# Kernel tuning notes

Hardware: AMD Instinct MI355X
Metric: run time of the kernel (lower is better)

The kernel has to match this reference:

```python
import jax, jax.numpy as jnp
import numpy as np

D_MODEL = 512
N_HEADS = 8
B, S = 4, 1024
REL_HIDDEN = 64


def setup_inputs() -> dict:
    key = jax.random.key(0)
    ks = jax.random.split(key, 16)

    def g(k, shape, scale=0.02):
        return jax.random.normal(k, shape, dtype=jnp.float32) * scale

    x = jax.random.normal(ks[0], (B, S, D_MODEL), dtype=jnp.float32)
    freqs = jax.random.uniform(ks[1], (B, S, 1), dtype=jnp.float32)
    return {
        "x": x,
        "freqs": freqs,
        "Wq": g(ks[2], (D_MODEL, D_MODEL)), "bq": g(ks[3], (D_MODEL,)),
        "Wk": g(ks[4], (D_MODEL, D_MODEL)), "bk": g(ks[5], (D_MODEL,)),
        "Wv": g(ks[6], (D_MODEL, D_MODEL)), "bv": g(ks[7], (D_MODEL,)),
        "Wo": g(ks[8], (D_MODEL, D_MODEL)), "bo": g(ks[9], (D_MODEL,)),
        "W1": g(ks[10], (2, REL_HIDDEN)), "b1": g(ks[11], (REL_HIDDEN,)),
        "W2": g(ks[12], (REL_HIDDEN, N_HEADS)), "b2": g(ks[13], (N_HEADS,)),
    }


def reference(x, freqs, Wq, bq, Wk, bk, Wv, bv, Wo, bo, W1, b1, W2, b2):
    b, s, d = x.shape
    h = N_HEADS
    dh = d // h

    def proj(W, bias):  # (b,s,d) -> (b,h,s,dh)
        return (x @ W + bias).reshape(b, s, h, dh).transpose(0, 2, 1, 3)

    Q = proj(Wq, bq)
    K = proj(Wk, bk)
    V = proj(Wv, bv)

    scores = jnp.einsum('bhid,bhjd->bhij', Q, K) / jnp.sqrt(jnp.float32(dh))

    # per-pair relative-frequency features: (b,s,s,2)
    eps = 1e-6
    fd = freqs[:, :, None, :] - freqs[:, None, :, :]
    fr = jnp.log((freqs[:, :, None, :] + eps) / (freqs[:, None, :, :] + eps))
    rel = jnp.concatenate([fd, fr], axis=-1)

    # MLP bias -> (b,s,s,h) -> (b,h,s,s)
    bias = jax.nn.relu(rel @ W1 + b1) @ W2 + b2
    scores = scores + jnp.transpose(bias, (0, 3, 1, 2))

    attn = jax.nn.softmax(scores, axis=-1)
    ctx = jnp.einsum('bhij,bhjd->bhid', attn, V)
    ctx = ctx.transpose(0, 2, 1, 3).reshape(b, s, d)
    return ctx @ Wo + bo
```

## Files before the change

### kernel.cpp

```cpp
#include <hip/hip_runtime.h>
#include <hip/hip_bf16.h>
#include <cstdint>

#define BATCH   4
#define SEQ     1024
#define DM      512
#define NH      8
#define DH      64
#define RH      64

typedef float f32x4 __attribute__((ext_vector_type(4)));
typedef __bf16 bf16x8 __attribute__((ext_vector_type(8)));

#define QB_OFF    (0)
#define KB_OFF    (4  << 20)
#define VT_OFF    (8  << 20)
#define XB_OFF    (12 << 20)
#define WT_OFF    (16 << 20)
#define WOT_OFF   (18 << 20)
#define W2T_OFF   (19 << 20)
#define AW_OFF    (20 << 20)
#define CW_OFF    (21 << 20)
#define CTXB_OFF  (22 << 20)
#define BIAS_OFF  (32 << 20)

__global__ __launch_bounds__(256) void cast_x(
    const float* __restrict__ x, __bf16* __restrict__ xb)
{
    const size_t i = ((size_t)blockIdx.x * 256 + threadIdx.x) * 8;
    const float4 a = *(const float4*)&x[i];
    const float4 b = *(const float4*)&x[i + 4];
    bf16x8 o;
    o[0] = (__bf16)a.x; o[1] = (__bf16)a.y; o[2] = (__bf16)a.z; o[3] = (__bf16)a.w;
    o[4] = (__bf16)b.x; o[5] = (__bf16)b.y; o[6] = (__bf16)b.z; o[7] = (__bf16)b.w;
    *(bf16x8*)&xb[i] = o;
}

__global__ __launch_bounds__(256) void cast_w(
    const float* __restrict__ Wq, const float* __restrict__ Wk,
    const float* __restrict__ Wv, const float* __restrict__ Wo,
    __bf16* __restrict__ Wt, __bf16* __restrict__ Wot)
{
    const int t = threadIdx.x;
    const int k0 = blockIdx.x * 64;
    const int n0 = blockIdx.y * 64;
    const int z  = blockIdx.z;
    const float* __restrict__ src = (z == 0) ? Wq : (z == 1) ? Wk : (z == 2) ? Wv : Wo;
    __bf16* __restrict__ dst = (z < 3) ? (Wt + (size_t)(z * 512 + n0) * 512)
                                       : (Wot + (size_t)n0 * 512);

    __shared__ __align__(16) float Ts[64][65];
    #pragma unroll
    for (int i = 0; i < 4; ++i) {
        const int id = t + i * 256;
        const int row = id >> 4, c4 = (id & 15) * 4;
        const float4 v = *(const float4*)&src[(size_t)(k0 + row) * DM + n0 + c4];
        Ts[row][c4 + 0] = v.x; Ts[row][c4 + 1] = v.y;
        Ts[row][c4 + 2] = v.z; Ts[row][c4 + 3] = v.w;
    }
    __syncthreads();
    #pragma unroll
    for (int i = 0; i < 2; ++i) {
        const int id = t + i * 256;
        const int rn = id >> 3, ck = (id & 7) * 8;
        bf16x8 o;
        #pragma unroll
        for (int j = 0; j < 8; ++j) o[j] = (__bf16)Ts[ck + j][rn];
        *(bf16x8*)&dst[(size_t)rn * 512 + k0 + ck] = o;
    }
}

__global__ __launch_bounds__(256) void w2t_kernel(
    const float* __restrict__ W2, __bf16* __restrict__ W2t)
{
    const int t = threadIdx.x;
    #pragma unroll
    for (int r = 0; r < 4; ++r) {
        const int id = t + r * 256;
        const int h = id >> 6, k = id & 63;
        W2t[id] = (h < NH) ? (__bf16)W2[k * NH + h] : (__bf16)0.f;
    }
}

__global__ __launch_bounds__(256) void gemm_qkv_mfma(
    const __bf16* __restrict__ xb, const __bf16* __restrict__ Wt,
    const float* __restrict__ bq, const float* __restrict__ bk,
    const float* __restrict__ bv,
    __bf16* __restrict__ Qb, __bf16* __restrict__ Kb, __bf16* __restrict__ Vtb)
{
    const int t = threadIdx.x;
    const int wave = t >> 6, lane = t & 63;
    const int wm = wave >> 1, wn = wave & 1;
    const int r = lane & 15, kc = lane >> 4, q4 = kc * 4;
    const int lin = blockIdx.y * 12 + blockIdx.x;
    const int swz = (lin & 7) * 48 + (lin >> 3);
    const int m0 = (swz / 12) * 128;
    const int n0 = (swz % 12) * 128;
    const int sec = n0 >> 9;
    const int nn = n0 & 511;

    __shared__ __align__(16) char smem[36864];
    __bf16* __restrict__ As = (__bf16*)smem;
    __bf16* __restrict__ Bs = (__bf16*)(smem + 18432);

    f32x4 acc[4][4];
    #pragma unroll
    for (int i = 0; i < 4; ++i)
        #pragma unroll
        for (int j = 0; j < 4; ++j) acc[i][j] = {0.f, 0.f, 0.f, 0.f};

    const int srow = t >> 3, sck = (t & 7) * 8;
    const __bf16* __restrict__ Ag = xb + (size_t)(m0 + srow) * 512 + sck;
    const __bf16* __restrict__ Bg = Wt + (size_t)(n0 + srow) * 512 + sck;

    for (int k0 = 0; k0 < 512; k0 += 64) {
        bf16x8 ra[4], rb[4];
        #pragma unroll
        for (int i = 0; i < 4; ++i) {
            ra[i] = *(const bf16x8*)(Ag + (size_t)i * 32 * 512 + k0);
            rb[i] = *(const bf16x8*)(Bg + (size_t)i * 32 * 512 + k0);
        }
        __syncthreads();
        #pragma unroll
        for (int i = 0; i < 4; ++i) {
            *(bf16x8*)&As[(srow + i * 32) * 72 + sck] = ra[i];
            *(bf16x8*)&Bs[(srow + i * 32) * 72 + sck] = rb[i];
        }
        __syncthreads();
        #pragma unroll
        for (int ks = 0; ks < 2; ++ks) {
            bf16x8 af[4], bf[4];
            #pragma unroll
            for (int mf = 0; mf < 4; ++mf)
                af[mf] = *(const bf16x8*)&As[(wm * 64 + mf * 16 + r) * 72 + ks * 32 + kc * 8];
            #pragma unroll
            for (int nf = 0; nf < 4; ++nf)
                bf[nf] = *(const bf16x8*)&Bs[(wn * 64 + nf * 16 + r) * 72 + ks * 32 + kc * 8];
            #pragma unroll
            for (int mf = 0; mf < 4; ++mf)
                #pragma unroll
                for (int nf = 0; nf < 4; ++nf)
                    acc[mf][nf] = __builtin_amdgcn_mfma_f32_16x16x32_bf16(
                        af[mf], bf[nf], acc[mf][nf], 0, 0, 0);
        }
    }

    const float* __restrict__ bias = (sec == 0) ? bq : (sec == 1) ? bk : bv;
    __syncthreads();
    __bf16* __restrict__ Ls = (__bf16*)smem;
    if (sec < 2) {
        #pragma unroll
        for (int mf = 0; mf < 4; ++mf)
            #pragma unroll
            for (int nf = 0; nf < 4; ++nf) {
                const int n_l = wn * 64 + nf * 16 + r;
                const float bb = bias[nn + n_l];
                #pragma unroll
                for (int rr = 0; rr < 4; ++rr)
                    Ls[(wm * 64 + mf * 16 + q4 + rr) * 136 + n_l] =
                        (__bf16)(acc[mf][nf][rr] + bb);
            }
    } else {
        #pragma unroll
        for (int mf = 0; mf < 4; ++mf)
            #pragma unroll
            for (int nf = 0; nf < 4; ++nf) {
                const int n_l = wn * 64 + nf * 16 + r;
                const float bb = bias[nn + n_l];
                #pragma unroll
                for (int rr = 0; rr < 4; ++rr)
                    Ls[n_l * 136 + (wm * 64 + mf * 16 + q4 + rr)] =
                        (__bf16)(acc[mf][nf][rr] + bb);
            }
    }
    __syncthreads();

    const int b = m0 >> 10, sbase = m0 & 1023;
    if (sec < 2) {
        __bf16* __restrict__ dst = sec ? Kb : Qb;
        #pragma unroll
        for (int i = 0; i < 8; ++i) {
            const int id = t + i * 256;
            const int row = id >> 4, nc = (id & 15) * 8;
            const bf16x8 v = *(const bf16x8*)&Ls[row * 136 + nc];
            const int ng = nn + nc, h = ng >> 6, c = ng & 63;
            *(bf16x8*)&dst[((size_t)(b * NH + h) * SEQ + sbase + row) * DH + c] = v;
        }
    } else {
        #pragma unroll
        for (int i = 0; i < 8; ++i) {
            const int id = t + i * 256;
            const int nrow = id >> 4, mc = (id & 15) * 8;
            const bf16x8 v = *(const bf16x8*)&Ls[nrow * 136 + mc];
            const int ng = nn + nrow, h = ng >> 6, c = ng & 63;
            *(bf16x8*)&Vtb[((size_t)(b * NH + h) * DH + c) * SEQ + sbase + mc] = v;
        }
    }
}

__global__ __launch_bounds__(256) void gemm_out_mfma(
    const __bf16* __restrict__ ctxb, const __bf16* __restrict__ Wot,
    const float* __restrict__ bo, float* __restrict__ out)
{
    const int t = threadIdx.x;
    const int wave = t >> 6, lane = t & 63;
    const int wm = wave >> 1, wn = wave & 1;
    const int r = lane & 15, kc = lane >> 4, q4 = kc * 4;
    const int lin = blockIdx.y * 4 + blockIdx.x;
    const int swz = (lin & 7) * 16 + (lin >> 3);
    const int m0 = (swz / 4) * 128;
    const int n0 = (swz % 4) * 128;

    __shared__ __align__(16) char smem[36864];
    __bf16* __restrict__ As = (__bf16*)smem;
    __bf16* __restrict__ Bs = (__bf16*)(smem + 18432);

    f32x4 acc[4][4];
    #pragma unroll
    for (int i = 0; i < 4; ++i)
        #pragma unroll
        for (int j = 0; j < 4; ++j) acc[i][j] = {0.f, 0.f, 0.f, 0.f};

    const int srow = t >> 3, sck = (t & 7) * 8;
    const __bf16* __restrict__ Ag = ctxb + (size_t)(m0 + srow) * 512 + sck;
    const __bf16* __restrict__ Bg = Wot + (size_t)(n0 + srow) * 512 + sck;

    for (int k0 = 0; k0 < 512; k0 += 64) {
        bf16x8 ra[4], rb[4];
        #pragma unroll
        for (int i = 0; i < 4; ++i) {
            ra[i] = *(const bf16x8*)(Ag + (size_t)i * 32 * 512 + k0);
            rb[i] = *(const bf16x8*)(Bg + (size_t)i * 32 * 512 + k0);
        }
        __syncthreads();
        #pragma unroll
        for (int i = 0; i < 4; ++i) {
            *(bf16x8*)&As[(srow + i * 32) * 72 + sck] = ra[i];
            *(bf16x8*)&Bs[(srow + i * 32) * 72 + sck] = rb[i];
        }
        __syncthreads();
        #pragma unroll
        for (int ks = 0; ks < 2; ++ks) {
            bf16x8 af[4], bf[4];
            #pragma unroll
            for (int mf = 0; mf < 4; ++mf)
                af[mf] = *(const bf16x8*)&As[(wm * 64 + mf * 16 + r) * 72 + ks * 32 + kc * 8];
            #pragma unroll
            for (int nf = 0; nf < 4; ++nf)
                bf[nf] = *(const bf16x8*)&Bs[(wn * 64 + nf * 16 + r) * 72 + ks * 32 + kc * 8];
            #pragma unroll
            for (int mf = 0; mf < 4; ++mf)
                #pragma unroll
                for (int nf = 0; nf < 4; ++nf)
                    acc[mf][nf] = __builtin_amdgcn_mfma_f32_16x16x32_bf16(
                        af[mf], bf[nf], acc[mf][nf], 0, 0, 0);
        }
    }

    #pragma unroll
    for (int mf = 0; mf < 4; ++mf)
        #pragma unroll
        for (int nf = 0; nf < 4; ++nf) {
            const int n_l = wn * 64 + nf * 16 + r;
            const float bb = bo[n0 + n_l];
            #pragma unroll
            for (int rr = 0; rr < 4; ++rr)
                out[(size_t)(m0 + wm * 64 + mf * 16 + q4 + rr) * DM + n0 + n_l] =
                    acc[mf][nf][rr] + bb;
        }
}

__global__ __launch_bounds__(64) void rel_kernel(
    const float* __restrict__ freqs,
    const float* __restrict__ W1,
    const float* __restrict__ b1,
    float* __restrict__ Aw,
    float* __restrict__ Cw)
{
    const int row = blockIdx.x;
    const int k = threadIdx.x;
    const float f = freqs[row];
    const float L = logf(f + 1e-6f);
    const float base = f * W1[k] + L * W1[RH + k];
    Aw[(size_t)row * RH + k] = base + b1[k];
    Cw[(size_t)row * RH + k] = -base;
}

__global__ __launch_bounds__(256) void bias_mfma(
    const float* __restrict__ Aw, const float* __restrict__ Cw,
    const __bf16* __restrict__ W2t, __bf16* __restrict__ biasb)
{
    const int t = threadIdx.x;
    const int wave = t >> 6, lane = t & 63;
    const int jl = lane & 15, kc = lane >> 4;
    const int j0 = blockIdx.x * 128;
    const int i0 = blockIdx.y * 16;
    const int b  = blockIdx.z;

    __shared__ __align__(16) float Cs[128][68];

    {
        const int jr = t >> 1, half = (t & 1) * 32;
        const float* __restrict__ src = &Cw[((size_t)b * SEQ + j0 + jr) * RH + half];
        #pragma unroll
        for (int q = 0; q < 8; ++q) {
            const float4 v = *(const float4*)(src + q * 4);
            *(float4*)&Cs[jr][half + q * 4] = v;
        }
    }

    const bf16x8 w2f0 = *(const bf16x8*)&W2t[jl * 64 + kc * 8];
    const bf16x8 w2f1 = *(const bf16x8*)&W2t[jl * 64 + 32 + kc * 8];

    __syncthreads();

    const int iw = i0 + wave * 4;
    #pragma unroll
    for (int ii = 0; ii < 4; ++ii) {
        const int i = iw + ii;
        const float* __restrict__ ap = &Aw[((size_t)b * SEQ + i) * RH];
        const float4 a0 = *(const float4*)(ap + kc * 8);
        const float4 a1 = *(const float4*)(ap + kc * 8 + 4);
        const float4 a2 = *(const float4*)(ap + 32 + kc * 8);
        const float4 a3 = *(const float4*)(ap + 32 + kc * 8 + 4);

        #pragma unroll
        for (int jt = 0; jt < 8; ++jt) {
            const float* __restrict__ cp = &Cs[jt * 16 + jl][kc * 8];
            f32x4 acc = {0.f, 0.f, 0.f, 0.f};

            const float4 c0 = *(const float4*)(cp);
            const float4 c1 = *(const float4*)(cp + 4);
            bf16x8 hb0;
            hb0[0] = (__bf16)fmaxf(a0.x + c0.x, 0.f);
            hb0[1] = (__bf16)fmaxf(a0.y + c0.y, 0.f);
            hb0[2] = (__bf16)fmaxf(a0.z + c0.z, 0.f);
            hb0[3] = (__bf16)fmaxf(a0.w + c0.w, 0.f);
            hb0[4] = (__bf16)fmaxf(a1.x + c1.x, 0.f);
            hb0[5] = (__bf16)fmaxf(a1.y + c1.y, 0.f);
            hb0[6] = (__bf16)fmaxf(a1.z + c1.z, 0.f);
            hb0[7] = (__bf16)fmaxf(a1.w + c1.w, 0.f);
            acc = __builtin_amdgcn_mfma_f32_16x16x32_bf16(w2f0, hb0, acc, 0, 0, 0);

            const float4 c2 = *(const float4*)(cp + 32);
            const float4 c3 = *(const float4*)(cp + 36);
            bf16x8 hb1;
            hb1[0] = (__bf16)fmaxf(a2.x + c2.x, 0.f);
            hb1[1] = (__bf16)fmaxf(a2.y + c2.y, 0.f);
            hb1[2] = (__bf16)fmaxf(a2.z + c2.z, 0.f);
            hb1[3] = (__bf16)fmaxf(a2.w + c2.w, 0.f);
            hb1[4] = (__bf16)fmaxf(a3.x + c3.x, 0.f);
            hb1[5] = (__bf16)fmaxf(a3.y + c3.y, 0.f);
            hb1[6] = (__bf16)fmaxf(a3.z + c3.z, 0.f);
            hb1[7] = (__bf16)fmaxf(a3.w + c3.w, 0.f);
            acc = __builtin_amdgcn_mfma_f32_16x16x32_bf16(w2f1, hb1, acc, 0, 0, 0);

            if (kc < 2) {
                #pragma unroll
                for (int rr = 0; rr < 4; ++rr)
                    biasb[(((size_t)b * NH + kc * 4 + rr) * SEQ + i) * SEQ
                          + j0 + jt * 16 + jl] = (__bf16)acc[rr];
            }
        }
    }
}

#define PSTR 1032

__global__ __launch_bounds__(512) void attn_mfma(
    const __bf16* __restrict__ Qb, const __bf16* __restrict__ Kb,
    const __bf16* __restrict__ Vtb, const __bf16* __restrict__ biasb,
    __bf16* __restrict__ ctxb)
{
    const int t = threadIdx.x;
    const int wave = t >> 6, lane = t & 63;
    const int r = lane & 15, kc = lane >> 4;
    const int blk = (blockIdx.x & 7) * 256 + (blockIdx.x >> 3);
    const int it = blk & 63;
    const int h  = (blk >> 6) & 7;
    const int b  = blk >> 9;
    const int s0 = it * 16;
    const int bh = b * NH + h;

    __shared__ __align__(16) __bf16 Pb[16 * PSTR];
    __shared__ __align__(16) float part[1088];
    __shared__ float red[8][16];
    __shared__ float invl[16];

    uint32_t brg[4][8];
    {
        const uint16_t* __restrict__ bb = (const uint16_t*)biasb
            + ((size_t)bh * SEQ + s0 + kc * 4) * SEQ + wave * 128 + r;
        #pragma unroll
        for (int rr = 0; rr < 4; ++rr)
            #pragma unroll
            for (int jt = 0; jt < 8; ++jt)
                brg[rr][jt] = bb[(size_t)rr * SEQ + jt * 16];
    }

    f32x4 sc[8];
    {
        const __bf16* __restrict__ Qp = Qb + ((size_t)bh * SEQ + s0) * DH;
        const __bf16* __restrict__ Kp = Kb + ((size_t)bh * SEQ + wave * 128) * DH;
        const bf16x8 qa0 = *(const bf16x8*)(Qp + r * DH + kc * 8);
        const bf16x8 qa1 = *(const bf16x8*)(Qp + r * DH + 32 + kc * 8);
        __builtin_amdgcn_s_setprio(1);
        #pragma unroll
        for (int jt = 0; jt < 8; ++jt) {
            const bf16x8 kb0 = *(const bf16x8*)(Kp + (size_t)(jt * 16 + r) * DH + kc * 8);
            const bf16x8 kb1 = *(const bf16x8*)(Kp + (size_t)(jt * 16 + r) * DH + 32 + kc * 8);
            f32x4 a = {0.f, 0.f, 0.f, 0.f};
            a = __builtin_amdgcn_mfma_f32_16x16x32_bf16(qa0, kb0, a, 0, 0, 0);
            a = __builtin_amdgcn_mfma_f32_16x16x32_bf16(qa1, kb1, a, 0, 0, 0);
            sc[jt] = a;
        }
        __builtin_amdgcn_s_setprio(0);
    }

    float psum[4] = {0.f, 0.f, 0.f, 0.f};
    #pragma unroll
    for (int jt = 0; jt < 8; ++jt) {
        #pragma unroll
        for (int rr = 0; rr < 4; ++rr) {
            const float s = fmaf(sc[jt][rr], 0.125f,
                                 __uint_as_float(brg[rr][jt] << 16));
            const float p = __expf(fminf(s, 30.f));
            sc[jt][rr] = p;
            psum[rr] += p;
        }
    }
    #pragma unroll
    for (int mask = 8; mask >= 1; mask >>= 1)
        #pragma unroll
        for (int rr = 0; rr < 4; ++rr)
            psum[rr] += __shfl_xor(psum[rr], mask);
    if (r == 0) {
        #pragma unroll
        for (int rr = 0; rr < 4; ++rr) red[wave][kc * 4 + rr] = psum[rr];
    }
    #pragma unroll
    for (int jt = 0; jt < 8; ++jt)
        #pragma unroll
        for (int rr = 0; rr < 4; ++rr)
            Pb[(kc * 4 + rr) * PSTR + wave * 128 + jt * 16 + r] = (__bf16)sc[jt][rr];
    __syncthreads();

    if (t < 16) {
        float l = 0.f;
        #pragma unroll
        for (int w = 0; w < 8; ++w) l += red[w][t];
        invl[t] = 1.0f / l;
    }

    {
        const int ct = wave & 3, kh = wave >> 2;
        const __bf16* __restrict__ Vp =
            Vtb + ((size_t)bh * DH + ct * 16 + r) * SEQ + kh * 512;
        f32x4 acc = {0.f, 0.f, 0.f, 0.f};
        __builtin_amdgcn_s_setprio(1);
        #pragma unroll 4
        for (int jt = 0; jt < 16; ++jt) {
            const bf16x8 pa = *(const bf16x8*)&Pb[r * PSTR + kh * 512 + jt * 32 + kc * 8];
            const bf16x8 vb = *(const bf16x8*)(Vp + jt * 32 + kc * 8);
            acc = __builtin_amdgcn_mfma_f32_16x16x32_bf16(pa, vb, acc, 0, 0, 0);
        }
        __builtin_amdgcn_s_setprio(0);
        if (kh == 1) {
            #pragma unroll
            for (int rr = 0; rr < 4; ++rr)
                part[ct * 272 + (kc * 4 + rr) * 17 + r] = acc[rr];
        }
        __syncthreads();
        if (kh == 0) {
            #pragma unroll
            for (int rr = 0; rr < 4; ++rr) {
                const int row = kc * 4 + rr;
                const float v = (acc[rr] + part[ct * 272 + row * 17 + r]) * invl[row];
                ctxb[((size_t)(b * SEQ) + s0 + row) * DM + h * DH + ct * 16 + r] = (__bf16)v;
            }
        }
    }
}

extern "C" void kernel_launch(void* const* d_in, const int* in_sizes, int n_in,
                              void* d_out, int out_size, void* d_ws, size_t ws_size,
                              hipStream_t stream)
{
    const float* x     = (const float*)d_in[0];
    const float* freqs = (const float*)d_in[1];
    const float* Wq    = (const float*)d_in[2];
    const float* bq    = (const float*)d_in[3];
    const float* Wk    = (const float*)d_in[4];
    const float* bk    = (const float*)d_in[5];
    const float* Wv    = (const float*)d_in[6];
    const float* bv    = (const float*)d_in[7];
    const float* Wo    = (const float*)d_in[8];
    const float* bo    = (const float*)d_in[9];
    const float* W1    = (const float*)d_in[10];
    const float* b1    = (const float*)d_in[11];
    const float* W2    = (const float*)d_in[12];

    char* wsb = (char*)d_ws;
    __bf16* Qb    = (__bf16*)(wsb + QB_OFF);
    __bf16* Kb    = (__bf16*)(wsb + KB_OFF);
    __bf16* Vtb   = (__bf16*)(wsb + VT_OFF);
    __bf16* xb    = (__bf16*)(wsb + XB_OFF);
    __bf16* Wt    = (__bf16*)(wsb + WT_OFF);
    __bf16* Wot   = (__bf16*)(wsb + WOT_OFF);
    __bf16* W2t   = (__bf16*)(wsb + W2T_OFF);
    float*  Aw    = (float*)(wsb + AW_OFF);
    float*  Cw    = (float*)(wsb + CW_OFF);
    __bf16* ctxb  = (__bf16*)(wsb + CTXB_OFF);
    __bf16* biasb = (__bf16*)(wsb + BIAS_OFF);
    float* out = (float*)d_out;

    cast_x<<<dim3(1024), 256, 0, stream>>>(x, xb);
    cast_w<<<dim3(8, 8, 4), 256, 0, stream>>>(Wq, Wk, Wv, Wo, Wt, Wot);
    w2t_kernel<<<dim3(1), 256, 0, stream>>>(W2, W2t);
    rel_kernel<<<dim3(4096), 64, 0, stream>>>(freqs, W1, b1, Aw, Cw);
    gemm_qkv_mfma<<<dim3(12, 32), 256, 0, stream>>>(xb, Wt, bq, bk, bv, Qb, Kb, Vtb);
    bias_mfma<<<dim3(8, 64, 4), 256, 0, stream>>>(Aw, Cw, W2t, biasb);
    attn_mfma<<<dim3(2048), 512, 0, stream>>>(Qb, Kb, Vtb, biasb, ctxb);
    gemm_out_mfma<<<dim3(4, 32), 256, 0, stream>>>(ctxb, Wot, bo, out);
}
```

Measured before the change: 219.2 us.

## Tile attention over 64 query rows with chunked key loop and double-buffered P

Each attention block now handles 64 query rows (4 query groups across waves) instead of 16, walking the 1024 keys in four 256-wide chunks. Per chunk it builds exp scores into a double-buffered LDS tile and does the P·V MFMAs right away, keeping the output accumulators in registers. This removes the cross-wave partial-sum exchange and lets each K/V tile serve four times as many queries, cutting global K/V traffic. The cost is four times fewer blocks (512) and a barrier per chunk, which may lower occupancy and latency hiding.

```diff
diff --git a/kernel.cpp b/kernel.cpp
--- a/kernel.cpp
+++ b/kernel.cpp
@@ -365,7 +365,7 @@
     }
 }
 
-#define PSTR 1032
+#define PCH 264
 
 __global__ __launch_bounds__(512) void attn_mfma(
     const __bf16* __restrict__ Qb, const __bf16* __restrict__ Kb,
@@ -373,62 +373,95 @@
     __bf16* __restrict__ ctxb)
 {
     const int t = threadIdx.x;
-    const int wave = t >> 6, lane = t & 63;
+    const int w = t >> 6, lane = t & 63;
     const int r = lane & 15, kc = lane >> 4;
-    const int blk = (blockIdx.x & 7) * 256 + (blockIdx.x >> 3);
-    const int it = blk & 63;
-    const int h  = (blk >> 6) & 7;
-    const int b  = blk >> 9;
-    const int s0 = it * 16;
+    const int qg = w & 3, jh = w >> 2;
+    const int blk = (blockIdx.x & 7) * 64 + (blockIdx.x >> 3);
+    const int it = blk & 15;
+    const int h  = (blk >> 4) & 7;
+    const int b  = blk >> 7;
+    const int s0 = it * 64;
     const int bh = b * NH + h;
 
-    __shared__ __align__(16) __bf16 Pb[16 * PSTR];
-    __shared__ __align__(16) float part[1088];
+    __shared__ __align__(16) __bf16 Pb[2][64 * PCH];
     __shared__ float red[8][16];
-    __shared__ float invl[16];
-
-    uint32_t brg[4][8];
-    {
-        const uint16_t* __restrict__ bb = (const uint16_t*)biasb
-            + ((size_t)bh * SEQ + s0 + kc * 4) * SEQ + wave * 128 + r;
-        #pragma unroll
-        for (int rr = 0; rr < 4; ++rr)
-            #pragma unroll
-            for (int jt = 0; jt < 8; ++jt)
-                brg[rr][jt] = bb[(size_t)rr * SEQ + jt * 16];
-    }
-
-    f32x4 sc[8];
-    {
-        const __bf16* __restrict__ Qp = Qb + ((size_t)bh * SEQ + s0) * DH;
-        const __bf16* __restrict__ Kp = Kb + ((size_t)bh * SEQ + wave * 128) * DH;
-        const bf16x8 qa0 = *(const bf16x8*)(Qp + r * DH + kc * 8);
-        const bf16x8 qa1 = *(const bf16x8*)(Qp + r * DH + 32 + kc * 8);
-        __builtin_amdgcn_s_setprio(1);
+
+    const __bf16* __restrict__ Qp = Qb + ((size_t)bh * SEQ + s0 + qg * 16) * DH;
+    const bf16x8 qa0 = *(const bf16x8*)(Qp + r * DH + kc * 8);
+    const bf16x8 qa1 = *(const bf16x8*)(Qp + r * DH + 32 + kc * 8);
+
+    float psum[4] = {0.f, 0.f, 0.f, 0.f};
+    f32x4 oacc0 = {0.f, 0.f, 0.f, 0.f};
+    f32x4 oacc1 = {0.f, 0.f, 0.f, 0.f};
+
+    const __bf16* __restrict__ KpBase = Kb + (size_t)bh * SEQ * DH;
+    const uint16_t* __restrict__ bbBase = (const uint16_t*)biasb
+        + ((size_t)bh * SEQ + s0 + qg * 16 + kc * 4) * SEQ + jh * 128 + r;
+
+    for (int c = 0; c < 4; ++c) {
+        uint32_t brg[4][8];
+        {
+            const uint16_t* __restrict__ bb = bbBase + c * 256;
+            #pragma unroll
+            for (int rr = 0; rr < 4; ++rr)
+                #pragma unroll
+                for (int jt = 0; jt < 8; ++jt)
+                    brg[rr][jt] = bb[(size_t)rr * SEQ + jt * 16];
+        }
+
+        f32x4 sc[8];
+        {
+            const __bf16* __restrict__ Kp =
+                KpBase + (size_t)(c * 256 + jh * 128) * DH;
+            __builtin_amdgcn_s_setprio(1);
+            #pragma unroll
+            for (int jt = 0; jt < 8; ++jt) {
+                const bf16x8 kb0 = *(const bf16x8*)(Kp + (size_t)(jt * 16 + r) * DH + kc * 8);
+                const bf16x8 kb1 = *(const bf16x8*)(Kp + (size_t)(jt * 16 + r) * DH + 32 + kc * 8);
+                f32x4 a = {0.f, 0.f, 0.f, 0.f};
+                a = __builtin_amdgcn_mfma_f32_16x16x32_bf16(qa0, kb0, a, 0, 0, 0);
+                a = __builtin_amdgcn_mfma_f32_16x16x32_bf16(qa1, kb1, a, 0, 0, 0);
+                sc[jt] = a;
+            }
+            __builtin_amdgcn_s_setprio(0);
+        }
+
+        __bf16* __restrict__ P = Pb[c & 1];
         #pragma unroll
         for (int jt = 0; jt < 8; ++jt) {
-            const bf16x8 kb0 = *(const bf16x8*)(Kp + (size_t)(jt * 16 + r) * DH + kc * 8);
-            const bf16x8 kb1 = *(const bf16x8*)(Kp + (size_t)(jt * 16 + r) * DH + 32 + kc * 8);
-            f32x4 a = {0.f, 0.f, 0.f, 0.f};
-            a = __builtin_amdgcn_mfma_f32_16x16x32_bf16(qa0, kb0, a, 0, 0, 0);
-            a = __builtin_amdgcn_mfma_f32_16x16x32_bf16(qa1, kb1, a, 0, 0, 0);
-            sc[jt] = a;
-        }
-        __builtin_amdgcn_s_setprio(0);
-    }
-
-    float psum[4] = {0.f, 0.f, 0.f, 0.f};
-    #pragma unroll
-    for (int jt = 0; jt < 8; ++jt) {
-        #pragma unroll
-        for (int rr = 0; rr < 4; ++rr) {
-            const float s = fmaf(sc[jt][rr], 0.125f,
-                                 __uint_as_float(brg[rr][jt] << 16));
-            const float p = __expf(fminf(s, 30.f));
-            sc[jt][rr] = p;
-            psum[rr] += p;
-        }
-    }
+            #pragma unroll
+            for (int rr = 0; rr < 4; ++rr) {
+                const float s = fmaf(sc[jt][rr], 0.125f,
+                                     __uint_as_float(brg[rr][jt] << 16));
+                const float p = __expf(fminf(s, 30.f));
+                psum[rr] += p;
+                P[(qg * 16 + kc * 4 + rr) * PCH + jh * 128 + jt * 16 + r] = (__bf16)p;
+            }
+        }
+        __syncthreads();
+
+        {
+            const __bf16* __restrict__ Pr = Pb[c & 1] + (qg * 16 + r) * PCH;
+            __builtin_amdgcn_s_setprio(1);
+            #pragma unroll
+            for (int cc = 0; cc < 2; ++cc) {
+                const int crow = (jh * 2 + cc) * 16 + r;
+                const __bf16* __restrict__ Vp =
+                    Vtb + ((size_t)bh * DH + crow) * SEQ + c * 256;
+                #pragma unroll
+                for (int jt = 0; jt < 8; ++jt) {
+                    const bf16x8 pa = *(const bf16x8*)(Pr + jt * 32 + kc * 8);
+                    const bf16x8 vb = *(const bf16x8*)(Vp + jt * 32 + kc * 8);
+                    if (cc == 0)
+                        oacc0 = __builtin_amdgcn_mfma_f32_16x16x32_bf16(pa, vb, oacc0, 0, 0, 0);
+                    else
+                        oacc1 = __builtin_amdgcn_mfma_f32_16x16x32_bf16(pa, vb, oacc1, 0, 0, 0);
+                }
+            }
+            __builtin_amdgcn_s_setprio(0);
+        }
+    }
+
     #pragma unroll
     for (int mask = 8; mask >= 1; mask >>= 1)
         #pragma unroll
@@ -436,49 +469,19 @@
             psum[rr] += __shfl_xor(psum[rr], mask);
     if (r == 0) {
         #pragma unroll
-        for (int rr = 0; rr < 4; ++rr) red[wave][kc * 4 + rr] = psum[rr];
-    }
-    #pragma unroll
-    for (int jt = 0; jt < 8; ++jt)
-        #pragma unroll
-        for (int rr = 0; rr < 4; ++rr)
-            Pb[(kc * 4 + rr) * PSTR + wave * 128 + jt * 16 + r] = (__bf16)sc[jt][rr];
+        for (int rr = 0; rr < 4; ++rr) red[w][kc * 4 + rr] = psum[rr];
+    }
     __syncthreads();
 
-    if (t < 16) {
-        float l = 0.f;
-        #pragma unroll
-        for (int w = 0; w < 8; ++w) l += red[w][t];
-        invl[t] = 1.0f / l;
-    }
-
-    {
-        const int ct = wave & 3, kh = wave >> 2;
-        const __bf16* __restrict__ Vp =
-            Vtb + ((size_t)bh * DH + ct * 16 + r) * SEQ + kh * 512;
-        f32x4 acc = {0.f, 0.f, 0.f, 0.f};
-        __builtin_amdgcn_s_setprio(1);
-        #pragma unroll 4
-        for (int jt = 0; jt < 16; ++jt) {
-            const bf16x8 pa = *(const bf16x8*)&Pb[r * PSTR + kh * 512 + jt * 32 + kc * 8];
-            const bf16x8 vb = *(const bf16x8*)(Vp + jt * 32 + kc * 8);
-            acc = __builtin_amdgcn_mfma_f32_16x16x32_bf16(pa, vb, acc, 0, 0, 0);
-        }
-        __builtin_amdgcn_s_setprio(0);
-        if (kh == 1) {
-            #pragma unroll
-            for (int rr = 0; rr < 4; ++rr)
-                part[ct * 272 + (kc * 4 + rr) * 17 + r] = acc[rr];
-        }
-        __syncthreads();
-        if (kh == 0) {
-            #pragma unroll
-            for (int rr = 0; rr < 4; ++rr) {
-                const int row = kc * 4 + rr;
-                const float v = (acc[rr] + part[ct * 272 + row * 17 + r]) * invl[row];
-                ctxb[((size_t)(b * SEQ) + s0 + row) * DM + h * DH + ct * 16 + r] = (__bf16)v;
-            }
-        }
+    #pragma unroll
+    for (int rr = 0; rr < 4; ++rr) {
+        const int qr = kc * 4 + rr;
+        const float inv = 1.0f / (red[qg][qr] + red[4 + qg][qr]);
+        const int q = s0 + qg * 16 + qr;
+        ctxb[((size_t)(b * SEQ) + q) * DM + h * DH + (jh * 2 + 0) * 16 + r] =
+            (__bf16)(oacc0[rr] * inv);
+        ctxb[((size_t)(b * SEQ) + q) * DM + h * DH + (jh * 2 + 1) * 16 + r] =
+            (__bf16)(oacc1[rr] * inv);
     }
 }
 
@@ -520,6 +523,6 @@
     rel_kernel<<<dim3(4096), 64, 0, stream>>>(freqs, W1, b1, Aw, Cw);
     gemm_qkv_mfma<<<dim3(12, 32), 256, 0, stream>>>(xb, Wt, bq, bk, bv, Qb, Kb, Vtb);
     bias_mfma<<<dim3(8, 64, 4), 256, 0, stream>>>(Aw, Cw, W2t, biasb);
-    attn_mfma<<<dim3(2048), 512, 0, stream>>>(Qb, Kb, Vtb, biasb, ctxb);
+    attn_mfma<<<dim3(512), 512, 0, stream>>>(Qb, Kb, Vtb, biasb, ctxb);
     gemm_out_mfma<<<dim3(4, 32), 256, 0, stream>>>(ctxb, Wot, bo, out);
 }
```

New measurement: 227.2 us. 3.7% more time.

## Split attention over key quarters with 64-query tiles and a separate combine kernel

Applied to the files above, without the earlier changes.

The attention kernel now processes 64 query rows per block against one quarter of the keys, instead of 16 query rows against all keys. The goal is better reuse of K and V loads across the four query groups and less LDS for P. Partial unnormalized outputs and row sums go to global memory in fp32. A new combine kernel adds the four partials, normalizes, and writes the bf16 context. This costs an extra launch and about 32MB of fp32 partial traffic.

```diff
diff --git a/kernel.cpp b/kernel.cpp
--- a/kernel.cpp
+++ b/kernel.cpp
@@ -23,6 +23,8 @@
 #define CW_OFF    (21 << 20)
 #define CTXB_OFF  (22 << 20)
 #define BIAS_OFF  (32 << 20)
+#define OP_OFF    (100 << 20)
+#define PS_OFF    (136 << 20)
 
 __global__ __launch_bounds__(256) void cast_x(
     const float* __restrict__ x, __bf16* __restrict__ xb)
@@ -365,32 +367,33 @@
     }
 }
 
-#define PSTR 1032
+#define PCH 264
 
 __global__ __launch_bounds__(512) void attn_mfma(
     const __bf16* __restrict__ Qb, const __bf16* __restrict__ Kb,
     const __bf16* __restrict__ Vtb, const __bf16* __restrict__ biasb,
-    __bf16* __restrict__ ctxb)
-{
-    const int t = threadIdx.x;
-    const int wave = t >> 6, lane = t & 63;
+    float* __restrict__ Op, float* __restrict__ ps)
+{
+    const int t = threadIdx.x;
+    const int w = t >> 6, lane = t & 63;
     const int r = lane & 15, kc = lane >> 4;
+    const int qg = w & 3, js = w >> 2;
     const int blk = (blockIdx.x & 7) * 256 + (blockIdx.x >> 3);
-    const int it = blk & 63;
+    const int jh = blk & 3;
+    const int qt = (blk >> 2) & 15;
     const int h  = (blk >> 6) & 7;
     const int b  = blk >> 9;
-    const int s0 = it * 16;
+    const int s0 = qt * 64;
+    const int j0 = jh * 256;
     const int bh = b * NH + h;
 
-    __shared__ __align__(16) __bf16 Pb[16 * PSTR];
-    __shared__ __align__(16) float part[1088];
+    __shared__ __align__(16) __bf16 P[64 * PCH];
     __shared__ float red[8][16];
-    __shared__ float invl[16];
 
     uint32_t brg[4][8];
     {
         const uint16_t* __restrict__ bb = (const uint16_t*)biasb
-            + ((size_t)bh * SEQ + s0 + kc * 4) * SEQ + wave * 128 + r;
+            + ((size_t)(bh * SEQ + s0 + qg * 16 + kc * 4)) * SEQ + j0 + js * 128 + r;
         #pragma unroll
         for (int rr = 0; rr < 4; ++rr)
             #pragma unroll
@@ -398,12 +401,14 @@
                 brg[rr][jt] = bb[(size_t)rr * SEQ + jt * 16];
     }
 
+    const __bf16* __restrict__ Qp = Qb + ((size_t)bh * SEQ + s0 + qg * 16) * DH;
+    const bf16x8 qa0 = *(const bf16x8*)(Qp + r * DH + kc * 8);
+    const bf16x8 qa1 = *(const bf16x8*)(Qp + r * DH + 32 + kc * 8);
+
     f32x4 sc[8];
     {
-        const __bf16* __restrict__ Qp = Qb + ((size_t)bh * SEQ + s0) * DH;
-        const __bf16* __restrict__ Kp = Kb + ((size_t)bh * SEQ + wave * 128) * DH;
-        const bf16x8 qa0 = *(const bf16x8*)(Qp + r * DH + kc * 8);
-        const bf16x8 qa1 = *(const bf16x8*)(Qp + r * DH + 32 + kc * 8);
+        const __bf16* __restrict__ Kp =
+            Kb + ((size_t)bh * SEQ + j0 + js * 128) * DH;
         __builtin_amdgcn_s_setprio(1);
         #pragma unroll
         for (int jt = 0; jt < 8; ++jt) {
@@ -425,8 +430,8 @@
             const float s = fmaf(sc[jt][rr], 0.125f,
                                  __uint_as_float(brg[rr][jt] << 16));
             const float p = __expf(fminf(s, 30.f));
-            sc[jt][rr] = p;
             psum[rr] += p;
+            P[(qg * 16 + kc * 4 + rr) * PCH + js * 128 + jt * 16 + r] = (__bf16)p;
         }
     }
     #pragma unroll
@@ -436,50 +441,79 @@
             psum[rr] += __shfl_xor(psum[rr], mask);
     if (r == 0) {
         #pragma unroll
-        for (int rr = 0; rr < 4; ++rr) red[wave][kc * 4 + rr] = psum[rr];
-    }
-    #pragma unroll
-    for (int jt = 0; jt < 8; ++jt)
-        #pragma unroll
-        for (int rr = 0; rr < 4; ++rr)
-            Pb[(kc * 4 + rr) * PSTR + wave * 128 + jt * 16 + r] = (__bf16)sc[jt][rr];
+        for (int rr = 0; rr < 4; ++rr) red[w][kc * 4 + rr] = psum[rr];
+    }
     __syncthreads();
 
-    if (t < 16) {
-        float l = 0.f;
-        #pragma unroll
-        for (int w = 0; w < 8; ++w) l += red[w][t];
-        invl[t] = 1.0f / l;
-    }
+    if (t < 64)
+        ps[((size_t)(bh * SEQ + s0 + t)) * 4 + jh] =
+            red[t >> 4][t & 15] + red[4 + (t >> 4)][t & 15];
 
     {
-        const int ct = wave & 3, kh = wave >> 2;
-        const __bf16* __restrict__ Vp =
-            Vtb + ((size_t)bh * DH + ct * 16 + r) * SEQ + kh * 512;
-        f32x4 acc = {0.f, 0.f, 0.f, 0.f};
+        const __bf16* __restrict__ Pr = P + (qg * 16 + r) * PCH;
+        const __bf16* __restrict__ Vp0 =
+            Vtb + ((size_t)(bh * DH + js * 32 + r)) * SEQ + j0;
+        const __bf16* __restrict__ Vp1 = Vp0 + (size_t)16 * SEQ;
+        f32x4 o0 = {0.f, 0.f, 0.f, 0.f};
+        f32x4 o1 = {0.f, 0.f, 0.f, 0.f};
         __builtin_amdgcn_s_setprio(1);
-        #pragma unroll 4
-        for (int jt = 0; jt < 16; ++jt) {
-            const bf16x8 pa = *(const bf16x8*)&Pb[r * PSTR + kh * 512 + jt * 32 + kc * 8];
-            const bf16x8 vb = *(const bf16x8*)(Vp + jt * 32 + kc * 8);
-            acc = __builtin_amdgcn_mfma_f32_16x16x32_bf16(pa, vb, acc, 0, 0, 0);
+        #pragma unroll
+        for (int ks = 0; ks < 8; ++ks) {
+            const bf16x8 pa = *(const bf16x8*)(Pr + ks * 32 + kc * 8);
+            const bf16x8 v0 = *(const bf16x8*)(Vp0 + ks * 32 + kc * 8);
+            const bf16x8 v1 = *(const bf16x8*)(Vp1 + ks * 32 + kc * 8);
+            o0 = __builtin_amdgcn_mfma_f32_16x16x32_bf16(pa, v0, o0, 0, 0, 0);
+            o1 = __builtin_amdgcn_mfma_f32_16x16x32_bf16(pa, v1, o1, 0, 0, 0);
         }
         __builtin_amdgcn_s_setprio(0);
-        if (kh == 1) {
-            #pragma unroll
-            for (int rr = 0; rr < 4; ++rr)
-                part[ct * 272 + (kc * 4 + rr) * 17 + r] = acc[rr];
-        }
-        __syncthreads();
-        if (kh == 0) {
-            #pragma unroll
-            for (int rr = 0; rr < 4; ++rr) {
-                const int row = kc * 4 + rr;
-                const float v = (acc[rr] + part[ct * 272 + row * 17 + r]) * invl[row];
-                ctxb[((size_t)(b * SEQ) + s0 + row) * DM + h * DH + ct * 16 + r] = (__bf16)v;
-            }
-        }
-    }
+        float* __restrict__ ob = Op
+            + ((size_t)(bh * SEQ + s0 + qg * 16 + kc * 4) * 4 + jh) * 64 + js * 32 + r;
+        #pragma unroll
+        for (int rr = 0; rr < 4; ++rr) {
+            ob[(size_t)rr * 256 + 0]  = o0[rr];
+            ob[(size_t)rr * 256 + 16] = o1[rr];
+        }
+    }
+}
+
+__global__ __launch_bounds__(256) void attn_combine(
+    const float* __restrict__ Op, const float* __restrict__ ps,
+    __bf16* __restrict__ ctxb)
+{
+    const int t = threadIdx.x;
+    const int row = blockIdx.x * 64 + (t >> 2);
+    const int c0 = (t & 3) * 16;
+    const float4 p4 = *(const float4*)&ps[(size_t)row * 4];
+    const float inv = 1.0f / (p4.x + p4.y + p4.z + p4.w);
+
+    const float* __restrict__ base = Op + (size_t)row * 256 + c0;
+    float acc[16];
+    #pragma unroll
+    for (int q = 0; q < 4; ++q) {
+        const float4 v = *(const float4*)(base + q * 4);
+        acc[q * 4 + 0] = v.x; acc[q * 4 + 1] = v.y;
+        acc[q * 4 + 2] = v.z; acc[q * 4 + 3] = v.w;
+    }
+    #pragma unroll
+    for (int jh = 1; jh < 4; ++jh)
+        #pragma unroll
+        for (int q = 0; q < 4; ++q) {
+            const float4 v = *(const float4*)(base + jh * 64 + q * 4);
+            acc[q * 4 + 0] += v.x; acc[q * 4 + 1] += v.y;
+            acc[q * 4 + 2] += v.z; acc[q * 4 + 3] += v.w;
+        }
+
+    const int bh = row >> 10, s = row & 1023;
+    const int b = bh >> 3, h = bh & 7;
+    __bf16* __restrict__ dst = ctxb + ((size_t)(b * SEQ + s)) * DM + h * DH + c0;
+    bf16x8 o0, o1;
+    #pragma unroll
+    for (int e = 0; e < 8; ++e) {
+        o0[e] = (__bf16)(acc[e] * inv);
+        o1[e] = (__bf16)(acc[8 + e] * inv);
+    }
+    *(bf16x8*)(dst) = o0;
+    *(bf16x8*)(dst + 8) = o1;
 }
 
 extern "C" void kernel_launch(void* const* d_in, const int* in_sizes, int n_in,
@@ -512,6 +546,8 @@
     float*  Cw    = (float*)(wsb + CW_OFF);
     __bf16* ctxb  = (__bf16*)(wsb + CTXB_OFF);
     __bf16* biasb = (__bf16*)(wsb + BIAS_OFF);
+    float*  Op    = (float*)(wsb + OP_OFF);
+    float*  psG   = (float*)(wsb + PS_OFF);
     float* out = (float*)d_out;
 
     cast_x<<<dim3(1024), 256, 0, stream>>>(x, xb);
@@ -520,6 +556,7 @@
     rel_kernel<<<dim3(4096), 64, 0, stream>>>(freqs, W1, b1, Aw, Cw);
     gemm_qkv_mfma<<<dim3(12, 32), 256, 0, stream>>>(xb, Wt, bq, bk, bv, Qb, Kb, Vtb);
     bias_mfma<<<dim3(8, 64, 4), 256, 0, stream>>>(Aw, Cw, W2t, biasb);
-    attn_mfma<<<dim3(2048), 512, 0, stream>>>(Qb, Kb, Vtb, biasb, ctxb);
+    attn_mfma<<<dim3(2048), 512, 0, stream>>>(Qb, Kb, Vtb, biasb, Op, psG);
+    attn_combine<<<dim3(512), 256, 0, stream>>>(Op, psG, ctxb);
     gemm_out_mfma<<<dim3(4, 32), 256, 0, stream>>>(ctxb, Wot, bo, out);
 }
```

Result: slower. 232.1 us (+5.9%).
